# Optimization experiments

Hardware: AMD Instinct MI355X
Metric: run time of the kernel (lower is better)

The kernel has to match this reference:

```python
import jax, jax.numpy as jnp
import numpy as np

# Llama-2-7B-like GQA attention, prefill over packed equal-length sequences
H = 4096      # hidden_size
NH = 32       # num_attention_heads
NKV = 8       # num_key_value_heads
HD = H // NH  # head_dim = 128
B = 4         # number of packed sequences
S = 1024      # seq_len per sequence
T = B * S     # total packed tokens
BASE = 10000.0  # rope_theta


def setup_inputs() -> dict:
    key = jax.random.key(0)
    ks = jax.random.split(key, 5)
    x = jax.random.normal(ks[0], (T, H), jnp.float32)
    positions = jnp.tile(jnp.arange(S, dtype=jnp.int32), B)  # per-seq positions
    kv_cache = jnp.zeros((1,), jnp.float32)  # placeholder (prefill: kv from current tokens)
    init = 0.02
    wq = jax.random.normal(ks[1], (NH * HD, H), jnp.float32) * init
    wk = jax.random.normal(ks[2], (NKV * HD, H), jnp.float32) * init
    wv = jax.random.normal(ks[3], (NKV * HD, H), jnp.float32) * init
    wo = jax.random.normal(ks[4], (H, NH * HD), jnp.float32) * init
    return {"x": x, "positions": positions, "kv_cache": kv_cache,
            "wq": wq, "wk": wk, "wv": wv, "wo": wo, "seq_len": S}


def _rope(xh, cos_b, sin_b):
    # xh: [T, Hh, D]; cos_b/sin_b: [T, 1, D] (freqs repeat-interleaved by 2)
    half = xh.shape[-1] // 2
    x_rot = jnp.concatenate([-xh[..., half:], xh[..., :half]], axis=-1)
    return xh * cos_b + x_rot * sin_b


def reference(x, positions, kv_cache, wq, wk, wv, wo, seq_len):
    Tn = x.shape[0]
    q = (x @ wq.T).reshape(Tn, NH, HD)
    k = (x @ wk.T).reshape(Tn, NKV, HD)
    v = (x @ wv.T).reshape(Tn, NKV, HD)
    # GQA: repeat_interleave kv heads
    rep = NH // NKV
    k = jnp.repeat(k, rep, axis=1)
    v = jnp.repeat(v, rep, axis=1)
    # RoPE tables (faithful to _precompute_freqs/_rotary_embeddings)
    inv_freq = 1.0 / (BASE ** (jnp.arange(0, HD, 2, dtype=jnp.float32) / HD))
    t = jnp.arange(seq_len, dtype=jnp.float32)
    freqs = t[:, None] * inv_freq[None, :]            # [S, D/2]
    cos, sin = jnp.cos(freqs), jnp.sin(freqs)
    pos = jnp.clip(positions.astype(jnp.int32), 0, seq_len - 1)
    cos_b = jnp.repeat(cos[pos], 2, axis=-1)[:, None, :]  # [T,1,D]
    sin_b = jnp.repeat(sin[pos], 2, axis=-1)[:, None, :]
    q = _rope(q, cos_b, sin_b)
    k = _rope(k, cos_b, sin_b)
    # Paged attention (prefill): causal attention within each packed sequence
    Bn = Tn // seq_len
    qb = q.reshape(Bn, seq_len, NH, HD)
    kb = k.reshape(Bn, seq_len, NH, HD)
    vb = v.reshape(Bn, seq_len, NH, HD)
    scores = jnp.einsum('bqhd,bkhd->bhqk', qb, kb) * (HD ** -0.5)
    causal = jnp.tril(jnp.ones((seq_len, seq_len), bool))
    scores = jnp.where(causal[None, None], scores, -jnp.inf)
    probs = jax.nn.softmax(scores, axis=-1)
    out = jnp.einsum('bhqk,bkhd->bqhd', probs, vb).reshape(Tn, NH * HD)
    return out @ wo.T
```

## Files before the change

kernel.cpp:

```cpp
#include <hip/hip_runtime.h>
#include <hip/hip_bf16.h>
#include <math.h>

#define T_TOK 4096
#define HID   4096
#define NHQ   32
#define NKVH  8
#define HDIM  128
#define SEQ   1024
#define NBATCH 4

typedef __attribute__((ext_vector_type(8))) short bf16x8;
typedef __attribute__((ext_vector_type(4))) float f32x4;

__device__ __forceinline__ unsigned short f2bf(float f) {
  union { float f; unsigned int u; } x; x.f = f;
  unsigned int r = x.u + 0x7FFFu + ((x.u >> 16) & 1u);
  return (unsigned short)(r >> 16);
}

#define GLOAD_LDS16(gp, lp)                                                        \
  __builtin_amdgcn_global_load_lds(                                                \
      (__attribute__((address_space(1))) void*)(unsigned long long)(const void*)(gp), \
      (__attribute__((address_space(3))) void*)(unsigned long long)(const void*)(lp), \
      16, 0, 0)

__global__ __launch_bounds__(256) void cast_all_k(const float* __restrict__ x,
                                                  const float* __restrict__ wq,
                                                  const float* __restrict__ wk,
                                                  const float* __restrict__ wv,
                                                  const float* __restrict__ wo,
                                                  unsigned short* __restrict__ xb,
                                                  unsigned short* __restrict__ wqkv,
                                                  unsigned short* __restrict__ wob) {
  int i = blockIdx.x * 256 + threadIdx.x;
  const float* src; unsigned short* dst; int off;
  if (i < 4194304)       { src = x;  dst = xb;   off = i; }
  else if (i < 8388608)  { src = wq; dst = wqkv; off = i - 4194304; }
  else if (i < 9437184)  { src = wk; dst = wqkv + 16777216; off = i - 8388608; }
  else if (i < 10485760) { src = wv; dst = wqkv + 20971520; off = i - 9437184; }
  else                   { src = wo; dst = wob;  off = i - 10485760; }
  float4 f = ((const float4*)src)[off];
  ushort4 o;
  o.x = f2bf(f.x); o.y = f2bf(f.y); o.z = f2bf(f.z); o.w = f2bf(f.w);
  ((ushort4*)dst)[off] = o;
}

__global__ __launch_bounds__(512, 2) void gemm_qkv(const unsigned short* __restrict__ A,
                                                   const unsigned short* __restrict__ B,
                                                   const int* __restrict__ pos,
                                                   unsigned short* __restrict__ qr,
                                                   unsigned short* __restrict__ kr,
                                                   unsigned short* __restrict__ vbuf) {
  const int K = 4096, nt = 64;
  __shared__ unsigned short AS[3][16384];
  __shared__ unsigned short BS[3][8192];
  const int tid  = threadIdx.x;
  const int lane = tid & 63;
  const int wave = tid >> 6;
  const int m16  = lane & 15;
  const int quad = lane >> 4;
  const int wm   = wave >> 1;
  const int wn   = wave & 1;

  const int gx = 48;
  const int orig = blockIdx.y * gx + blockIdx.x;
  const int swz = (orig & 7) * 96 + (orig >> 3);
  const long rowBase = (long)(swz / gx) * 256;
  const long colBase = (long)(swz % gx) * 128;

  int aoff[2], boff[2];
#pragma unroll
  for (int ks = 0; ks < 2; ++ks) {
    int sx = ((ks * 4 + quad) ^ (m16 & 7)) * 8;
    aoff[ks] = (wm * 64 + m16) * 64 + sx;
    boff[ks] = (wn * 32 + m16) * 64 + sx;
  }

  const long Kl = K;
  const int sck = ((tid & 7) ^ ((tid >> 3) & 7)) * 8;
  const unsigned short* gA = A + (rowBase + (tid >> 3)) * Kl + sck;
  const unsigned short* gB = B + (colBase + (tid >> 3)) * Kl + sck;
  const int dofs = wave * 512;

#define STG_B(slot_, ko_) { GLOAD_LDS16(gB + (ko_),            &BS[slot_][dofs]);         \
                            GLOAD_LDS16(gB + (ko_) + 64 * Kl,  &BS[slot_][4096 + dofs]); }
#define STG_A(slot_, ko_) { GLOAD_LDS16(gA + (ko_),            &AS[slot_][dofs]);         \
                            GLOAD_LDS16(gA + (ko_) + 64 * Kl,  &AS[slot_][4096 + dofs]);  \
                            GLOAD_LDS16(gA + (ko_) + 128 * Kl, &AS[slot_][8192 + dofs]);  \
                            GLOAD_LDS16(gA + (ko_) + 192 * Kl, &AS[slot_][12288 + dofs]); }

  f32x4 acc[4][4] = {};

  STG_A(0, 0); STG_B(0, 0);
  STG_A(1, 64); STG_B(1, 64);
  asm volatile("s_waitcnt vmcnt(6)" ::: "memory");
  __builtin_amdgcn_s_barrier();

  for (int g = 0; g < 22; ++g) {
#pragma unroll
    for (int u = 0; u < 3; ++u) {
      const int t = g * 3 + u;
      if (t < nt) {
        const bool doStage = (t + 2) < nt;
        const long kn = (long)(t + 2) * 64;
        bf16x8 af[4], bfr[4];

#pragma unroll
        for (int mf = 0; mf < 4; ++mf)
          af[mf] = *(const bf16x8*)(&AS[u][aoff[0] + mf * 1024]);
#pragma unroll
        for (int nf = 0; nf < 4; ++nf)
          bfr[nf] = *(const bf16x8*)(&BS[u][boff[0] + (nf & 1) * 1024 + (nf >> 1) * 4096]);
        if (doStage) STG_A((u + 2) % 3, kn);
        __builtin_amdgcn_s_barrier();
        asm volatile("s_waitcnt lgkmcnt(0)" ::: "memory");
        __builtin_amdgcn_s_setprio(1);
#pragma unroll
        for (int mf = 0; mf < 4; ++mf)
#pragma unroll
          for (int nf = 0; nf < 4; ++nf)
            acc[mf][nf] = __builtin_amdgcn_mfma_f32_16x16x32_bf16(af[mf], bfr[nf], acc[mf][nf], 0, 0, 0);
        __builtin_amdgcn_s_setprio(0);
        __builtin_amdgcn_s_barrier();

#pragma unroll
        for (int mf = 0; mf < 4; ++mf)
          af[mf] = *(const bf16x8*)(&AS[u][aoff[1] + mf * 1024]);
#pragma unroll
        for (int nf = 0; nf < 4; ++nf)
          bfr[nf] = *(const bf16x8*)(&BS[u][boff[1] + (nf & 1) * 1024 + (nf >> 1) * 4096]);
        if (doStage) STG_B((u + 2) % 3, kn);
        __builtin_amdgcn_s_barrier();
        asm volatile("s_waitcnt lgkmcnt(0)" ::: "memory");
        __builtin_amdgcn_s_setprio(1);
#pragma unroll
        for (int mf = 0; mf < 4; ++mf)
#pragma unroll
          for (int nf = 0; nf < 4; ++nf)
            acc[mf][nf] = __builtin_amdgcn_mfma_f32_16x16x32_bf16(af[mf], bfr[nf], acc[mf][nf], 0, 0, 0);
        __builtin_amdgcn_s_setprio(0);
        if (doStage)         asm volatile("s_waitcnt vmcnt(6)" ::: "memory");
        else if (t + 1 < nt) asm volatile("s_waitcnt vmcnt(0)" ::: "memory");
        __builtin_amdgcn_s_barrier();
      }
    }
  }

  const int n0 = (int)colBase;
  unsigned short* dst;
  int rstride, colofs;
  bool dorope;
  if (n0 < 4096)       { dst = qr;   rstride = NHQ * HDIM;  colofs = n0;        dorope = true; }
  else if (n0 < 5120)  { dst = kr;   rstride = NKVH * HDIM; colofs = n0 - 4096; dorope = true; }
  else                 { dst = vbuf; rstride = NKVH * HDIM; colofs = n0 - 5120; dorope = false; }
  const float c0 = -13.287712379549449f / 64.0f;
  float fA[2], fB[2];
#pragma unroll
  for (int e = 0; e < 2; ++e) {
    int d = wn * 32 + e * 16 + m16;
    fA[e] = exp2f(c0 * (float)(d >> 1));
    fB[e] = exp2f(c0 * (float)((d >> 1) + 32));
  }
#pragma unroll
  for (int mf = 0; mf < 4; ++mf) {
#pragma unroll
    for (int reg = 0; reg < 4; ++reg) {
      int grow = (int)rowBase + wm * 64 + mf * 16 + quad * 4 + reg;
      unsigned short* drow = dst + (long)grow * rstride + colofs;
      if (dorope) {
        int p = pos[grow];
        p = p < 0 ? 0 : (p > SEQ - 1 ? SEQ - 1 : p);
        float pf = (float)p;
#pragma unroll
        for (int e = 0; e < 2; ++e) {
          int d = wn * 32 + e * 16 + m16;
          float lo = acc[mf][e][reg], hi = acc[mf][e + 2][reg];
          float s1, cc1, s2, cc2;
          __sincosf(pf * fA[e], &s1, &cc1);
          __sincosf(pf * fB[e], &s2, &cc2);
          drow[d]      = f2bf(lo * cc1 - hi * s1);
          drow[d + 64] = f2bf(hi * cc2 + lo * s2);
        }
      } else {
#pragma unroll
        for (int e = 0; e < 2; ++e) {
          int d = wn * 32 + e * 16 + m16;
          drow[d]      = f2bf(acc[mf][e][reg]);
          drow[d + 64] = f2bf(acc[mf][e + 2][reg]);
        }
      }
    }
  }
}

__global__ __launch_bounds__(512, 2) void gemm_o(const unsigned short* __restrict__ A,
                                                 const unsigned short* __restrict__ B,
                                                 float* __restrict__ C) {
  const int K = 4096, N = 4096, nt = 128;
  __shared__ unsigned short AS[3][8192];
  __shared__ unsigned short BS[3][8192];
  const int tid  = threadIdx.x;
  const int lane = tid & 63;
  const int wave = tid >> 6;
  const int m16  = lane & 15;
  const int quad = lane >> 4;
  const int wm   = wave >> 2;
  const int wn   = wave & 3;

  const int gx = 16;
  const int orig = blockIdx.y * gx + blockIdx.x;
  const int swz = (orig & 7) * 32 + (orig >> 3);
  const long rowBase = (long)(swz / gx) * 256;
  const long colBase = (long)(swz % gx) * 256;

  const int slot8 = ((quad + 4 * (m16 & 1)) ^ (m16 >> 1)) * 8;
  const int aob = (wm * 64 + (m16 >> 1)) * 64 + slot8;
  const int bob = (wn * 32 + (m16 >> 1)) * 64 + slot8;

  const long Kl = K;
  const int z = (tid & 7) ^ ((tid >> 3) & 7);
  const long srow = 2 * (tid >> 3) + (z >> 2);
  const int sk = (z & 3) * 8;
  const unsigned short* oA = A + (rowBase + srow) * Kl + sk;
  const unsigned short* oB = B + (colBase + srow) * Kl + sk;
  const int dofs = wave * 512;

#define OSTG_A(sl_, ko_) { GLOAD_LDS16(oA + (ko_),            &AS[sl_][dofs]);         \
                           GLOAD_LDS16(oA + (ko_) + 128 * Kl, &AS[sl_][4096 + dofs]); }
#define OSTG_B(sl_, ko_) { GLOAD_LDS16(oB + (ko_),            &BS[sl_][dofs]);         \
                           GLOAD_LDS16(oB + (ko_) + 128 * Kl, &BS[sl_][4096 + dofs]); }

  f32x4 acc[8][4] = {};

  OSTG_A(0, 0);  OSTG_B(0, 0);
  OSTG_A(1, 32); OSTG_B(1, 32);
  asm volatile("s_waitcnt vmcnt(4)" ::: "memory");
  __builtin_amdgcn_s_barrier();

  for (int g = 0; g < 43; ++g) {
#pragma unroll
    for (int u = 0; u < 3; ++u) {
      const int t = g * 3 + u;
      if (t < nt) {
        const bool doStage = (t + 2) < nt;
        const long kn = (long)(t + 2) * 32;
        bf16x8 af[4], bfr[4];

#pragma unroll
        for (int nf = 0; nf < 4; ++nf)
          bfr[nf] = *(const bf16x8*)(&BS[u][bob + nf * 512]);
#pragma unroll
        for (int mf = 0; mf < 4; ++mf)
          af[mf] = *(const bf16x8*)(&AS[u][aob + mf * 512]);
        if (doStage) OSTG_A((u + 2) % 3, kn);
        __builtin_amdgcn_s_barrier();
        asm volatile("s_waitcnt lgkmcnt(0)" ::: "memory");
        __builtin_amdgcn_s_setprio(1);
#pragma unroll
        for (int mf = 0; mf < 4; ++mf)
#pragma unroll
          for (int nf = 0; nf < 4; ++nf)
            acc[mf][nf] = __builtin_amdgcn_mfma_f32_16x16x32_bf16(af[mf], bfr[nf], acc[mf][nf], 0, 0, 0);
        __builtin_amdgcn_s_setprio(0);
        __builtin_amdgcn_s_barrier();

#pragma unroll
        for (int mf = 0; mf < 4; ++mf)
          af[mf] = *(const bf16x8*)(&AS[u][aob + (4 + mf) * 512]);
        if (doStage) OSTG_B((u + 2) % 3, kn);
        __builtin_amdgcn_s_barrier();
        asm volatile("s_waitcnt lgkmcnt(0)" ::: "memory");
        __builtin_amdgcn_s_setprio(1);
#pragma unroll
        for (int mf = 0; mf < 4; ++mf)
#pragma unroll
          for (int nf = 0; nf < 4; ++nf)
            acc[4 + mf][nf] = __builtin_amdgcn_mfma_f32_16x16x32_bf16(af[mf], bfr[nf], acc[4 + mf][nf], 0, 0, 0);
        __builtin_amdgcn_s_setprio(0);
        if (doStage)         asm volatile("s_waitcnt vmcnt(4)" ::: "memory");
        else if (t + 1 < nt) asm volatile("s_waitcnt vmcnt(0)" ::: "memory");
        __builtin_amdgcn_s_barrier();
      }
    }
  }

#pragma unroll
  for (int mf = 0; mf < 8; ++mf)
#pragma unroll
    for (int nf = 0; nf < 4; ++nf) {
      long c = colBase + wn * 64 + nf * 16 + m16;
#pragma unroll
      for (int reg = 0; reg < 4; ++reg) {
        long row = rowBase + wm * 128 + mf * 16 + quad * 4 + reg;
        C[row * N + c] = acc[mf][nf][reg];
      }
    }
}

#define ATT_SCALE_L2 0.12754227022f
__global__ __launch_bounds__(256) void attn_k(const unsigned short* __restrict__ Qp,
                                              const unsigned short* __restrict__ Kp,
                                              const unsigned short* __restrict__ Vp,
                                              unsigned short* __restrict__ Op) {
  const int pr = blockIdx.x, h = blockIdx.y, b = blockIdx.z;
  const int kvh = h >> 2;
  const int tid = threadIdx.x, wave = tid >> 6, lane = tid & 63;
  const int m16 = lane & 15, quad = lane >> 4;

  __shared__ unsigned short Ks[2][64][128];
  __shared__ unsigned short Vt[2][128][64];
  __shared__ unsigned short Ps[4][32][64];

  const unsigned short* Kh = Kp + (long)(b * SEQ) * (NKVH * HDIM) + kvh * HDIM;
  const unsigned short* Vh = Vp + (long)(b * SEQ) * (NKVH * HDIM) + kvh * HDIM;

#define STAGE_K(ktv, bufp) {                                               \
    _Pragma("unroll")                                                      \
    for (int it_ = 0; it_ < 4; ++it_) {                                    \
      int c_ = it_ * 256 + tid;                                            \
      int row_ = c_ >> 4, psg_ = c_ & 15;                                  \
      int sg_ = (psg_ & 8) | ((psg_ & 7) ^ (row_ & 7));                    \
      GLOAD_LDS16(Kh + ((long)(ktv) * 64 + row_) * (NKVH * HDIM) + sg_ * 8,\
                  ((unsigned short*)(bufp)) + (it_ * 256 + wave * 64) * 8);\
    } }

#define LOAD_V(ktv, dvv) {                                                 \
    _Pragma("unroll")                                                      \
    for (int it_ = 0; it_ < 4; ++it_)                                      \
      dvv[it_] = *(const uint4*)(Vh + ((long)(ktv) * 64 + lane) * (NKVH * HDIM) + (it_ * 4 + wave) * 8); }

#define SCATTER_V(bufp, dvv) {                                             \
    _Pragma("unroll")                                                      \
    for (int it_ = 0; it_ < 4; ++it_) {                                    \
      const unsigned short* pv_ = (const unsigned short*)&dvv[it_];        \
      int seg_ = it_ * 4 + wave;                                           \
      _Pragma("unroll")                                                    \
      for (int e_ = 0; e_ < 8; ++e_) {                                     \
        int d_ = seg_ * 8 + e_;                                            \
        (bufp)[d_][((((lane >> 3) + d_) & 7) * 8) + (lane & 7)] = pv_[e_]; \
      } } }

  for (int pass = 0; pass < 2; ++pass) {
    const int qt = pass ? pr : (7 - pr);
    const int qbase = qt * 128;
    const int wq_lo = qbase + wave * 32;

    bf16x8 qa[2][4];
#pragma unroll
    for (int i = 0; i < 2; ++i) {
      const unsigned short* qrow =
          Qp + (long)(b * SEQ + wq_lo + i * 16 + m16) * (NHQ * HDIM) + h * HDIM;
#pragma unroll
      for (int kk = 0; kk < 4; ++kk)
        qa[i][kk] = *(const bf16x8*)(qrow + kk * 32 + quad * 8);
    }

    f32x4 o[2][8] = {};
    float mrow[2][4], lrow[2][4];
#pragma unroll
    for (int i = 0; i < 2; ++i)
#pragma unroll
      for (int r = 0; r < 4; ++r) { mrow[i][r] = -1e30f; lrow[i][r] = 0.f; }

    const int nkt = qt * 2 + 2;

    {
      STAGE_K(0, Ks[0]);
      uint4 dv[4];
      LOAD_V(0, dv);
      asm volatile("s_waitcnt vmcnt(0)" ::: "memory");
      SCATTER_V(Vt[0], dv);
    }
    __syncthreads();

    for (int kt = 0; kt < nkt; ++kt) {
      const int cb = kt & 1;
      const bool active = (kt * 64) <= (wq_lo + 31);
      const bool more = (kt + 1) < nkt;

      f32x4 s4[2][4] = {};
      if (active) {
        __builtin_amdgcn_s_setprio(1);
#pragma unroll
        for (int kk = 0; kk < 4; ++kk) {
          bf16x8 kbf[4];
#pragma unroll
          for (int j = 0; j < 4; ++j) {
            int row = j * 16 + m16;
            int cl = kk * 4 + quad;
            int ps = (cl & 8) | ((cl & 7) ^ (row & 7));
            kbf[j] = *(const bf16x8*)(&Ks[cb][row][ps * 8]);
          }
#pragma unroll
          for (int i = 0; i < 2; ++i)
#pragma unroll
            for (int j = 0; j < 4; ++j)
              s4[i][j] = __builtin_amdgcn_mfma_f32_16x16x32_bf16(qa[i][kk], kbf[j], s4[i][j], 0, 0, 0);
        }
        __builtin_amdgcn_s_setprio(0);
      }

      uint4 dv[4];
      if (more) {
        STAGE_K(kt + 1, Ks[cb ^ 1]);
        LOAD_V(kt + 1, dv);
      }
      asm volatile("" ::: "memory");

      if (active) {
        const bool full = (kt * 64 + 63) <= wq_lo;
#pragma unroll
        for (int i = 0; i < 2; ++i) {
#pragma unroll
          for (int r = 0; r < 4; ++r) {
            const int qrow = i * 16 + quad * 4 + r;
            const int qi = qbase + wave * 32 + qrow;
            float v[4];
#pragma unroll
            for (int j = 0; j < 4; ++j) {
              v[j] = s4[i][j][r] * ATT_SCALE_L2;
              if (!full && (kt * 64 + j * 16 + m16 > qi)) v[j] = -1e30f;
            }
            float mx = fmaxf(fmaxf(v[0], v[1]), fmaxf(v[2], v[3]));
            mx = fmaxf(mx, __shfl_xor(mx, 1));
            mx = fmaxf(mx, __shfl_xor(mx, 2));
            mx = fmaxf(mx, __shfl_xor(mx, 4));
            mx = fmaxf(mx, __shfl_xor(mx, 8));
            float mold = mrow[i][r];
            float mnew = fmaxf(mold, mx);
            float alpha = exp2f(mold - mnew);
            float rs = 0.f;
#pragma unroll
            for (int j = 0; j < 4; ++j) {
              float pj = exp2f(v[j] - mnew);
              rs += pj;
              int col = j * 16 + m16;
              Ps[wave][qrow][((((col >> 3) + qrow) & 7) * 8) + (col & 7)] = f2bf(pj);
            }
            rs += __shfl_xor(rs, 1); rs += __shfl_xor(rs, 2);
            rs += __shfl_xor(rs, 4); rs += __shfl_xor(rs, 8);
            lrow[i][r] = lrow[i][r] * alpha + rs;
            mrow[i][r] = mnew;
#pragma unroll
            for (int n = 0; n < 8; ++n) o[i][n][r] *= alpha;
          }
        }
        __builtin_amdgcn_s_setprio(1);
#pragma unroll
        for (int kk = 0; kk < 2; ++kk) {
          bf16x8 pa[2], vb[8];
#pragma unroll
          for (int i = 0; i < 2; ++i) {
            int row = i * 16 + m16;
            pa[i] = *(const bf16x8*)(&Ps[wave][row][(((kk * 4 + quad) + row) & 7) * 8]);
          }
#pragma unroll
          for (int n = 0; n < 8; ++n) {
            int row = n * 16 + m16;
            vb[n] = *(const bf16x8*)(&Vt[cb][row][(((kk * 4 + quad) + row) & 7) * 8]);
          }
#pragma unroll
          for (int i = 0; i < 2; ++i)
#pragma unroll
            for (int n = 0; n < 8; ++n)
              o[i][n] = __builtin_amdgcn_mfma_f32_16x16x32_bf16(pa[i], vb[n], o[i][n], 0, 0, 0);
        }
        __builtin_amdgcn_s_setprio(0);
      }

      if (more) {
        asm volatile("s_waitcnt vmcnt(0)" ::: "memory");
        SCATTER_V(Vt[cb ^ 1], dv);
      }
      __syncthreads();
    }

#pragma unroll
    for (int i = 0; i < 2; ++i) {
#pragma unroll
      for (int r = 0; r < 4; ++r) {
        float inv = 1.0f / lrow[i][r];
        unsigned short* orow =
            Op + (long)(b * SEQ + wq_lo + i * 16 + quad * 4 + r) * (NHQ * HDIM) + h * HDIM;
#pragma unroll
        for (int n = 0; n < 8; ++n)
          orow[n * 16 + m16] = f2bf(o[i][n][r] * inv);
      }
    }
  }
}

extern "C" void kernel_launch(void* const* d_in, const int* in_sizes, int n_in,
                              void* d_out, int out_size, void* d_ws, size_t ws_size,
                              hipStream_t stream) {
  (void)in_sizes; (void)n_in; (void)out_size; (void)ws_size;
  const float* x  = (const float*)d_in[0];
  const int* pos  = (const int*)d_in[1];
  const float* wq = (const float*)d_in[3];
  const float* wk = (const float*)d_in[4];
  const float* wv = (const float*)d_in[5];
  const float* wo = (const float*)d_in[6];
  float* out = (float*)d_out;

  char* ws = (char*)d_ws;
  unsigned short* xb    = (unsigned short*)(ws);
  unsigned short* wqkv  = (unsigned short*)(ws + (32ll << 20));
  unsigned short* wob   = (unsigned short*)(ws + (80ll << 20));
  unsigned short* qr    = (unsigned short*)(ws + (112ll << 20));
  unsigned short* kr    = (unsigned short*)(ws + (144ll << 20));
  unsigned short* vb_   = (unsigned short*)(ws + (152ll << 20));
  unsigned short* ao    = (unsigned short*)(ws + (160ll << 20));

  cast_all_k<<<57344, 256, 0, stream>>>(x, wq, wk, wv, wo, xb, wqkv, wob);
  gemm_qkv<<<dim3(48, 16), 512, 0, stream>>>(xb, wqkv, pos, qr, kr, vb_);
  attn_k<<<dim3(4, 32, 4), 256, 0, stream>>>(qr, kr, vb_, ao);
  gemm_o<<<dim3(16, 16), 512, 0, stream>>>(ao, wob, out);
}
```

Before: 750.0 us.

## Restructure O-projection GEMM into quadrant k64 pipeline and widen attention blocks

Rewrites the output-projection GEMM to use k-step 64 with double-buffered A/B halves split into quadrants, interleaving loads and MFMAs across four sub-steps. The attention kernel moves from 4 to 8 waves per block (256-query tiles, half as many blocks) and adds a lazy softmax rescale that skips the alpha correction unless the max grows past a threshold. The row-sum reduction moves out of the inner loop to the end. The lazy rescale may risk exp overflow or precision loss within the threshold, and the change also halves the number of attention blocks.

```diff
diff --git a/kernel.cpp b/kernel.cpp
--- a/kernel.cpp
+++ b/kernel.cpp
@@ -194,115 +194,129 @@
   }
 }
 
-__global__ __launch_bounds__(512, 2) void gemm_o(const unsigned short* __restrict__ A,
-                                                 const unsigned short* __restrict__ B,
-                                                 float* __restrict__ C) {
-  const int K = 4096, N = 4096, nt = 128;
-  __shared__ unsigned short AS[3][8192];
-  __shared__ unsigned short BS[3][8192];
+__global__ __launch_bounds__(512, 1) void gemm_o8(const unsigned short* __restrict__ A,
+                                                  const unsigned short* __restrict__ B,
+                                                  float* __restrict__ C) {
+  const int K = 4096, nt = 64, N = 4096;
+  __shared__ unsigned short AS[2][2][128][64];
+  __shared__ unsigned short BS[2][2][128][64];
   const int tid  = threadIdx.x;
   const int lane = tid & 63;
   const int wave = tid >> 6;
   const int m16  = lane & 15;
   const int quad = lane >> 4;
-  const int wm   = wave >> 2;
-  const int wn   = wave & 3;
+  const int wm2  = wave >> 2;
+  const int wn2  = wave & 3;
 
   const int gx = 16;
+  const int nwg = 256;
   const int orig = blockIdx.y * gx + blockIdx.x;
-  const int swz = (orig & 7) * 32 + (orig >> 3);
+  const int swz = (orig & 7) * (nwg >> 3) + (orig >> 3);
   const long rowBase = (long)(swz / gx) * 256;
   const long colBase = (long)(swz % gx) * 256;
 
-  const int slot8 = ((quad + 4 * (m16 & 1)) ^ (m16 >> 1)) * 8;
-  const int aob = (wm * 64 + (m16 >> 1)) * 64 + slot8;
-  const int bob = (wn * 32 + (m16 >> 1)) * 64 + slot8;
+  int aof[2], bof[2];
+#pragma unroll
+  for (int ks = 0; ks < 2; ++ks) {
+    int sx = ((ks * 4 + quad) ^ (m16 & 7)) * 8;
+    aof[ks] = (wm2 * 64 + m16) * 64 + sx;
+    bof[ks] = (wn2 * 16 + m16) * 64 + sx;
+  }
 
   const long Kl = K;
-  const int z = (tid & 7) ^ ((tid >> 3) & 7);
-  const long srow = 2 * (tid >> 3) + (z >> 2);
-  const int sk = (z & 3) * 8;
-  const unsigned short* oA = A + (rowBase + srow) * Kl + sk;
-  const unsigned short* oB = B + (colBase + srow) * Kl + sk;
+  const int sck = ((tid & 7) ^ ((tid >> 3) & 7)) * 8;
+  const unsigned short* gA = A + (rowBase + (tid >> 3)) * Kl + sck;
+  const unsigned short* gB = B + (colBase + (tid >> 3)) * Kl + sck;
   const int dofs = wave * 512;
 
-#define OSTG_A(sl_, ko_) { GLOAD_LDS16(oA + (ko_),            &AS[sl_][dofs]);         \
-                           GLOAD_LDS16(oA + (ko_) + 128 * Kl, &AS[sl_][4096 + dofs]); }
-#define OSTG_B(sl_, ko_) { GLOAD_LDS16(oB + (ko_),            &BS[sl_][dofs]);         \
-                           GLOAD_LDS16(oB + (ko_) + 128 * Kl, &BS[sl_][4096 + dofs]); }
-
-  f32x4 acc[8][4] = {};
-
-  OSTG_A(0, 0);  OSTG_B(0, 0);
-  OSTG_A(1, 32); OSTG_B(1, 32);
-  asm volatile("s_waitcnt vmcnt(4)" ::: "memory");
+#define STGO(XS_, gX_, db_, hf_, ko_) {                                                      \
+    GLOAD_LDS16(gX_ + (long)((hf_) * 128) * Kl + (ko_),      ((unsigned short*)&XS_[db_][hf_][0][0]) + dofs);  \
+    GLOAD_LDS16(gX_ + (long)((hf_) * 128 + 64) * Kl + (ko_), ((unsigned short*)&XS_[db_][hf_][64][0]) + dofs); }
+
+#define RD_A(d_, qa_) {                                                   \
+    const unsigned short* Ah_ = &AS[d_][qa_][0][0];                       \
+    _Pragma("unroll") for (int mf = 0; mf < 4; ++mf)                      \
+      _Pragma("unroll") for (int ks = 0; ks < 2; ++ks)                    \
+        af[mf][ks] = *(const bf16x8*)(Ah_ + aof[ks] + mf * 1024); }
+
+#define RD_B(d_, qb_, dst_) {                                             \
+    const unsigned short* Bh_ = &BS[d_][qb_][0][0];                       \
+    _Pragma("unroll") for (int nf = 0; nf < 2; ++nf)                      \
+      _Pragma("unroll") for (int ks = 0; ks < 2; ++ks)                    \
+        dst_[nf][ks] = *(const bf16x8*)(Bh_ + bof[ks] + nf * 4096); }
+
+#define MFMA16(qa_, qb_, b_) {                                            \
+    _Pragma("unroll") for (int mf = 0; mf < 4; ++mf)                      \
+      _Pragma("unroll") for (int nf = 0; nf < 2; ++nf)                    \
+        _Pragma("unroll") for (int ks = 0; ks < 2; ++ks)                  \
+          acc[qa_][qb_][mf][nf] = __builtin_amdgcn_mfma_f32_16x16x32_bf16(\
+              af[mf][ks], b_[nf][ks], acc[qa_][qb_][mf][nf], 0, 0, 0); }
+
+  f32x4 acc[2][2][4][2] = {};
+  bf16x8 af[4][2], b0[2][2], b1[2][2];
+
+  STGO(AS, gA, 0, 0, 0);   STGO(BS, gB, 0, 1, 0);
+  STGO(AS, gA, 0, 1, 0);   STGO(BS, gB, 0, 0, 0);
+  STGO(AS, gA, 1, 0, 64);  STGO(BS, gB, 1, 1, 64);
+  STGO(AS, gA, 1, 1, 64);
+  asm volatile("s_waitcnt vmcnt(6)" ::: "memory");
   __builtin_amdgcn_s_barrier();
 
-  for (int g = 0; g < 43; ++g) {
-#pragma unroll
-    for (int u = 0; u < 3; ++u) {
-      const int t = g * 3 + u;
-      if (t < nt) {
-        const bool doStage = (t + 2) < nt;
-        const long kn = (long)(t + 2) * 32;
-        bf16x8 af[4], bfr[4];
-
-#pragma unroll
-        for (int nf = 0; nf < 4; ++nf)
-          bfr[nf] = *(const bf16x8*)(&BS[u][bob + nf * 512]);
-#pragma unroll
-        for (int mf = 0; mf < 4; ++mf)
-          af[mf] = *(const bf16x8*)(&AS[u][aob + mf * 512]);
-        if (doStage) OSTG_A((u + 2) % 3, kn);
-        __builtin_amdgcn_s_barrier();
-        asm volatile("s_waitcnt lgkmcnt(0)" ::: "memory");
-        __builtin_amdgcn_s_setprio(1);
-#pragma unroll
-        for (int mf = 0; mf < 4; ++mf)
-#pragma unroll
-          for (int nf = 0; nf < 4; ++nf)
-            acc[mf][nf] = __builtin_amdgcn_mfma_f32_16x16x32_bf16(af[mf], bfr[nf], acc[mf][nf], 0, 0, 0);
-        __builtin_amdgcn_s_setprio(0);
-        __builtin_amdgcn_s_barrier();
-
-#pragma unroll
-        for (int mf = 0; mf < 4; ++mf)
-          af[mf] = *(const bf16x8*)(&AS[u][aob + (4 + mf) * 512]);
-        if (doStage) OSTG_B((u + 2) % 3, kn);
-        __builtin_amdgcn_s_barrier();
-        asm volatile("s_waitcnt lgkmcnt(0)" ::: "memory");
-        __builtin_amdgcn_s_setprio(1);
-#pragma unroll
-        for (int mf = 0; mf < 4; ++mf)
-#pragma unroll
-          for (int nf = 0; nf < 4; ++nf)
-            acc[4 + mf][nf] = __builtin_amdgcn_mfma_f32_16x16x32_bf16(af[mf], bfr[nf], acc[4 + mf][nf], 0, 0, 0);
-        __builtin_amdgcn_s_setprio(0);
-        if (doStage)         asm volatile("s_waitcnt vmcnt(4)" ::: "memory");
-        else if (t + 1 < nt) asm volatile("s_waitcnt vmcnt(0)" ::: "memory");
-        __builtin_amdgcn_s_barrier();
-      }
-    }
-  }
-
-#pragma unroll
-  for (int mf = 0; mf < 8; ++mf)
-#pragma unroll
-    for (int nf = 0; nf < 4; ++nf) {
-      long c = colBase + wn * 64 + nf * 16 + m16;
-#pragma unroll
-      for (int reg = 0; reg < 4; ++reg) {
-        long row = rowBase + wm * 128 + mf * 16 + quad * 4 + reg;
-        C[row * N + c] = acc[mf][nf][reg];
-      }
-    }
+#define KSTEP(n_, d_) {                                                               \
+    RD_A(d_, 0); RD_B(d_, 0, b0);                                                     \
+    if ((n_) + 1 < nt) STGO(BS, gB, (d_) ^ 1, 0, ((n_) + 1) * 64);                    \
+    asm volatile("s_waitcnt lgkmcnt(8)" ::: "memory");                                \
+    __builtin_amdgcn_s_barrier();                                                     \
+    asm volatile("s_waitcnt lgkmcnt(0)" ::: "memory");                                \
+    __builtin_amdgcn_s_setprio(1); MFMA16(0, 0, b0); __builtin_amdgcn_s_setprio(0);   \
+    __builtin_amdgcn_s_barrier();                                                     \
+    RD_B(d_, 1, b1);                                                                  \
+    if ((n_) + 2 < nt) STGO(AS, gA, d_, 0, ((n_) + 2) * 64);                          \
+    __builtin_amdgcn_s_barrier();                                                     \
+    asm volatile("s_waitcnt lgkmcnt(0)" ::: "memory");                                \
+    __builtin_amdgcn_s_setprio(1); MFMA16(0, 1, b1); __builtin_amdgcn_s_setprio(0);   \
+    __builtin_amdgcn_s_barrier();                                                     \
+    RD_A(d_, 1);                                                                      \
+    if ((n_) + 2 < nt) STGO(BS, gB, d_, 1, ((n_) + 2) * 64);                          \
+    __builtin_amdgcn_s_barrier();                                                     \
+    asm volatile("s_waitcnt lgkmcnt(0)" ::: "memory");                                \
+    __builtin_amdgcn_s_setprio(1); MFMA16(1, 1, b1); __builtin_amdgcn_s_setprio(0);   \
+    __builtin_amdgcn_s_barrier();                                                     \
+    if ((n_) + 2 < nt) STGO(AS, gA, d_, 1, ((n_) + 2) * 64);                          \
+    __builtin_amdgcn_s_barrier();                                                     \
+    __builtin_amdgcn_s_setprio(1); MFMA16(1, 0, b0); __builtin_amdgcn_s_setprio(0);   \
+    if ((n_) + 2 < nt) asm volatile("s_waitcnt vmcnt(6)" ::: "memory");               \
+    else               asm volatile("s_waitcnt vmcnt(0)" ::: "memory");               \
+    __builtin_amdgcn_s_barrier(); }
+
+  for (int it = 0; it < 32; ++it) {
+    KSTEP(2 * it, 0);
+    KSTEP(2 * it + 1, 1);
+  }
+
+#pragma unroll
+  for (int qa = 0; qa < 2; ++qa)
+#pragma unroll
+    for (int qb = 0; qb < 2; ++qb)
+#pragma unroll
+      for (int mf = 0; mf < 4; ++mf)
+#pragma unroll
+        for (int nf = 0; nf < 2; ++nf) {
+          long c = colBase + qb * 128 + wn2 * 16 + nf * 64 + m16;
+#pragma unroll
+          for (int reg = 0; reg < 4; ++reg) {
+            long row = rowBase + qa * 128 + wm2 * 64 + mf * 16 + quad * 4 + reg;
+            C[row * N + c] = acc[qa][qb][mf][nf][reg];
+          }
+        }
 }
 
 #define ATT_SCALE_L2 0.12754227022f
-__global__ __launch_bounds__(256) void attn_k(const unsigned short* __restrict__ Qp,
-                                              const unsigned short* __restrict__ Kp,
-                                              const unsigned short* __restrict__ Vp,
-                                              unsigned short* __restrict__ Op) {
+#define RESCALE_THR 8.0f
+__global__ __launch_bounds__(512) void attn8(const unsigned short* __restrict__ Qp,
+                                             const unsigned short* __restrict__ Kp,
+                                             const unsigned short* __restrict__ Vp,
+                                             unsigned short* __restrict__ Op) {
   const int pr = blockIdx.x, h = blockIdx.y, b = blockIdx.z;
   const int kvh = h >> 2;
   const int tid = threadIdx.x, wave = tid >> 6, lane = tid & 63;
@@ -310,31 +324,31 @@
 
   __shared__ unsigned short Ks[2][64][128];
   __shared__ unsigned short Vt[2][128][64];
-  __shared__ unsigned short Ps[4][32][64];
+  __shared__ unsigned short Ps[8][32][64];
 
   const unsigned short* Kh = Kp + (long)(b * SEQ) * (NKVH * HDIM) + kvh * HDIM;
   const unsigned short* Vh = Vp + (long)(b * SEQ) * (NKVH * HDIM) + kvh * HDIM;
 
-#define STAGE_K(ktv, bufp) {                                               \
+#define STAGE_K8(ktv, bufp) {                                              \
     _Pragma("unroll")                                                      \
-    for (int it_ = 0; it_ < 4; ++it_) {                                    \
-      int c_ = it_ * 256 + tid;                                            \
+    for (int it_ = 0; it_ < 2; ++it_) {                                    \
+      int c_ = it_ * 512 + tid;                                            \
       int row_ = c_ >> 4, psg_ = c_ & 15;                                  \
       int sg_ = (psg_ & 8) | ((psg_ & 7) ^ (row_ & 7));                    \
       GLOAD_LDS16(Kh + ((long)(ktv) * 64 + row_) * (NKVH * HDIM) + sg_ * 8,\
-                  ((unsigned short*)(bufp)) + (it_ * 256 + wave * 64) * 8);\
+                  ((unsigned short*)(bufp)) + (it_ * 512 + wave * 64) * 8);\
     } }
 
-#define LOAD_V(ktv, dvv) {                                                 \
+#define LOAD_V8(ktv, dvv) {                                                \
     _Pragma("unroll")                                                      \
-    for (int it_ = 0; it_ < 4; ++it_)                                      \
-      dvv[it_] = *(const uint4*)(Vh + ((long)(ktv) * 64 + lane) * (NKVH * HDIM) + (it_ * 4 + wave) * 8); }
-
-#define SCATTER_V(bufp, dvv) {                                             \
+    for (int it_ = 0; it_ < 2; ++it_)                                      \
+      dvv[it_] = *(const uint4*)(Vh + ((long)(ktv) * 64 + lane) * (NKVH * HDIM) + (it_ * 8 + wave) * 8); }
+
+#define SCATTER_V8(bufp, dvv) {                                            \
     _Pragma("unroll")                                                      \
-    for (int it_ = 0; it_ < 4; ++it_) {                                    \
+    for (int it_ = 0; it_ < 2; ++it_) {                                    \
       const unsigned short* pv_ = (const unsigned short*)&dvv[it_];        \
-      int seg_ = it_ * 4 + wave;                                           \
+      int seg_ = it_ * 8 + wave;                                           \
       _Pragma("unroll")                                                    \
       for (int e_ = 0; e_ < 8; ++e_) {                                     \
         int d_ = seg_ * 8 + e_;                                            \
@@ -342,8 +356,8 @@
       } } }
 
   for (int pass = 0; pass < 2; ++pass) {
-    const int qt = pass ? pr : (7 - pr);
-    const int qbase = qt * 128;
+    const int qt = pass ? pr : (3 - pr);
+    const int qbase = qt * 256;
     const int wq_lo = qbase + wave * 32;
 
     bf16x8 qa[2][4];
@@ -363,14 +377,14 @@
 #pragma unroll
       for (int r = 0; r < 4; ++r) { mrow[i][r] = -1e30f; lrow[i][r] = 0.f; }
 
-    const int nkt = qt * 2 + 2;
+    const int nkt = (qt + 1) * 4;
 
     {
-      STAGE_K(0, Ks[0]);
-      uint4 dv[4];
-      LOAD_V(0, dv);
+      STAGE_K8(0, Ks[0]);
+      uint4 dv0[2];
+      LOAD_V8(0, dv0);
       asm volatile("s_waitcnt vmcnt(0)" ::: "memory");
-      SCATTER_V(Vt[0], dv);
+      SCATTER_V8(Vt[0], dv0);
     }
     __syncthreads();
 
@@ -401,10 +415,10 @@
         __builtin_amdgcn_s_setprio(0);
       }
 
-      uint4 dv[4];
+      uint4 dv[2];
       if (more) {
-        STAGE_K(kt + 1, Ks[cb ^ 1]);
-        LOAD_V(kt + 1, dv);
+        STAGE_K8(kt + 1, Ks[cb ^ 1]);
+        LOAD_V8(kt + 1, dv);
       }
       asm volatile("" ::: "memory");
 
@@ -428,8 +442,8 @@
             mx = fmaxf(mx, __shfl_xor(mx, 4));
             mx = fmaxf(mx, __shfl_xor(mx, 8));
             float mold = mrow[i][r];
-            float mnew = fmaxf(mold, mx);
-            float alpha = exp2f(mold - mnew);
+            bool skip = (mx <= mold + RESCALE_THR);
+            float mnew = skip ? mold : mx;
             float rs = 0.f;
 #pragma unroll
             for (int j = 0; j < 4; ++j) {
@@ -438,12 +452,14 @@
               int col = j * 16 + m16;
               Ps[wave][qrow][((((col >> 3) + qrow) & 7) * 8) + (col & 7)] = f2bf(pj);
             }
-            rs += __shfl_xor(rs, 1); rs += __shfl_xor(rs, 2);
-            rs += __shfl_xor(rs, 4); rs += __shfl_xor(rs, 8);
-            lrow[i][r] = lrow[i][r] * alpha + rs;
-            mrow[i][r] = mnew;
-#pragma unroll
-            for (int n = 0; n < 8; ++n) o[i][n][r] *= alpha;
+            if (!skip) {
+              float alpha = exp2f(mold - mnew);
+              lrow[i][r] *= alpha;
+#pragma unroll
+              for (int n = 0; n < 8; ++n) o[i][n][r] *= alpha;
+              mrow[i][r] = mnew;
+            }
+            lrow[i][r] += rs;
           }
         }
         __builtin_amdgcn_s_setprio(1);
@@ -471,7 +487,7 @@
 
       if (more) {
         asm volatile("s_waitcnt vmcnt(0)" ::: "memory");
-        SCATTER_V(Vt[cb ^ 1], dv);
+        SCATTER_V8(Vt[cb ^ 1], dv);
       }
       __syncthreads();
     }
@@ -480,7 +496,10 @@
     for (int i = 0; i < 2; ++i) {
 #pragma unroll
       for (int r = 0; r < 4; ++r) {
-        float inv = 1.0f / lrow[i][r];
+        float ls = lrow[i][r];
+        ls += __shfl_xor(ls, 1); ls += __shfl_xor(ls, 2);
+        ls += __shfl_xor(ls, 4); ls += __shfl_xor(ls, 8);
+        float inv = 1.0f / ls;
         unsigned short* orow =
             Op + (long)(b * SEQ + wq_lo + i * 16 + quad * 4 + r) * (NHQ * HDIM) + h * HDIM;
 #pragma unroll
@@ -514,6 +533,6 @@
 
   cast_all_k<<<57344, 256, 0, stream>>>(x, wq, wk, wv, wo, xb, wqkv, wob);
   gemm_qkv<<<dim3(48, 16), 512, 0, stream>>>(xb, wqkv, pos, qr, kr, vb_);
-  attn_k<<<dim3(4, 32, 4), 256, 0, stream>>>(qr, kr, vb_, ao);
-  gemm_o<<<dim3(16, 16), 512, 0, stream>>>(ao, wob, out);
+  attn8<<<dim3(2, 32, 4), 512, 0, stream>>>(qr, kr, vb_, ao);
+  gemm_o8<<<dim3(16, 16), 512, 0, stream>>>(ao, wob, out);
 }
```

Measured after the change: 657.1 us. 1.14x faster.
